# Kernel tuning notes

Measured on AMD Instinct MI355X. Metric: run time of the kernel, lower is better.

## Reference

```python
import jax, jax.numpy as jnp
import numpy as np

H = 16  # n_heads

def _rmsnorm(x, g, eps=1e-6):
    return x * jax.lax.rsqrt(jnp.mean(x * x, axis=-1, keepdims=True) + eps) * g

def _rope_diag(L, hd, dtype):
    # Diagonal of the full [L, hd, hd] rotary matrix: cos(pos * theta_pair) at every dim.
    # (The torch einsum 'bhld,ldd->bhld' extracts this diagonal, so no pairwise rotation occurs.)
    pair = jnp.arange(hd) // 2
    theta = 10000.0 ** (-2.0 * pair / hd)
    return jnp.cos(jnp.arange(L)[:, None].astype(jnp.float32) * theta[None, :]).astype(dtype)


def setup_inputs() -> dict:
    key = jax.random.key(0)
    ks = jax.random.split(key, 8)
    B, L, E = 2, 2048, 2048
    F = 2 * E  # SwiGLU width
    s = 0.02
    return {
        "x": jax.random.normal(ks[0], (B, L, E), jnp.float32),
        "g": jnp.ones((E,), jnp.float32),
        "wq": jax.random.normal(ks[1], (E, E), jnp.float32) * s,
        "wk": jax.random.normal(ks[2], (E, E), jnp.float32) * s,
        "wv": jax.random.normal(ks[3], (E, E), jnp.float32) * s,
        "w1": jax.random.normal(ks[4], (E, F), jnp.float32) * s,
        "b1": jnp.zeros((F,), jnp.float32),
        "wg": jax.random.normal(ks[5], (F, F), jnp.float32) * s,
        "bg": jnp.zeros((F,), jnp.float32),
        "wl": jax.random.normal(ks[6], (F, F), jnp.float32) * s,
        "bl": jnp.zeros((F,), jnp.float32),
        "beta": jnp.ones((1,), jnp.float32),
        "w2": jax.random.normal(ks[7], (F, E), jnp.float32) * s,
        "b2": jnp.zeros((E,), jnp.float32),
    }


def reference(x, g, wq, wk, wv, w1, b1, wg, bg, wl, bl, beta, w2, b2):
    B, L, E = x.shape
    hd = E // H
    x_res = x
    h = _rmsnorm(x, g)
    # projections -> [B, H, L, hd]
    q = (h @ wq).reshape(B, L, H, hd).transpose(0, 2, 1, 3)
    k = (h @ wk).reshape(B, L, H, hd).transpose(0, 2, 1, 3)
    v = (h @ wv).reshape(B, L, H, hd).transpose(0, 2, 1, 3)
    D = _rope_diag(L, hd, x.dtype)  # [L, hd], diagonal of rotary matrix
    q = q * D
    k = k * D
    score = jnp.einsum('bhld,bhmd->bhlm', q, k)  # [B,H,L,L]
    # causal mask added BEFORE scaling (faithful to source)
    mask = jnp.triu(jnp.full((L, L), -jnp.inf, dtype=score.dtype), k=1)
    score = (score + mask) / jnp.sqrt(jnp.asarray(hd, score.dtype))
    attn = jax.nn.softmax(score, axis=-1)
    o = jnp.einsum('bhlm,bhmd->bhld', attn, v)
    o = o.transpose(0, 2, 1, 3).reshape(B, L, E)
    x = o + x_res
    x_res = x
    h = _rmsnorm(x, g)
    h = h @ w1 + b1  # [B, L, 2E]
    gate = h @ wg + bg
    lin = h @ wl + bl
    act = gate * jax.nn.sigmoid(beta * gate) * lin
    out = act @ w2 + b2
    return out + x_res
```

## Files before the change

### kernel.cpp

```cpp
#include <hip/hip_runtime.h>
#include <cstdint>
#include <math.h>


typedef _Float16 f16;
typedef _Float16 f16x8 __attribute__((ext_vector_type(8)));
typedef _Float16 f16x4 __attribute__((ext_vector_type(4)));
typedef float    f32x4 __attribute__((ext_vector_type(4)));

#define MFMA_16x16x32(a, b, c) __builtin_amdgcn_mfma_f32_16x16x32_f16(a, b, c, 0, 0, 0)

__device__ __forceinline__ void gload_lds16(const void* g, void* lds) {
  __builtin_amdgcn_global_load_lds(
      (__attribute__((address_space(1))) void*)(uintptr_t)g,
      (__attribute__((address_space(3))) void*)(unsigned)(uintptr_t)lds,
      16, 0, 0);
}

__global__ void convT_k(const float* __restrict__ W, f16* __restrict__ Wt,
                        int K, int N) {
  __shared__ float tile[32][33];
  const int n0 = blockIdx.x << 5, k0 = blockIdx.y << 5;
  const int t = threadIdx.x;
  const int r = t >> 3, c4 = (t & 7) << 2;
  const f32x4 v = *(const f32x4*)(W + (size_t)(k0 + r) * N + n0 + c4);
  tile[r][c4 + 0] = v[0]; tile[r][c4 + 1] = v[1];
  tile[r][c4 + 2] = v[2]; tile[r][c4 + 3] = v[3];
  __syncthreads();
  f16x4 o;
  o[0] = (f16)tile[c4 + 0][r]; o[1] = (f16)tile[c4 + 1][r];
  o[2] = (f16)tile[c4 + 2][r]; o[3] = (f16)tile[c4 + 3][r];
  *(f16x4*)(Wt + (size_t)(n0 + r) * K + k0 + c4) = o;
}

__global__ void rope_tab_k(float* __restrict__ Dt) {
  const int l = blockIdx.x, d = threadIdx.x;
  const float th = __expf(-0.0719557841f * (float)(d & ~1));
  Dt[(l << 7) + d] = cosf((float)l * th);
}

__global__ void rmsnorm_k(const float* __restrict__ X, const float* __restrict__ G,
                          f16* __restrict__ H) {
  __shared__ float red[4];
  const int row = blockIdx.x, t = threadIdx.x;
  const float* xp = X + ((size_t)row << 11) + (t << 3);
  const f32x4 v0 = *(const f32x4*)xp;
  const f32x4 v1 = *(const f32x4*)(xp + 4);
  float ss = v0[0]*v0[0] + v0[1]*v0[1] + v0[2]*v0[2] + v0[3]*v0[3]
           + v1[0]*v1[0] + v1[1]*v1[1] + v1[2]*v1[2] + v1[3]*v1[3];
#pragma unroll
  for (int m = 1; m < 64; m <<= 1) ss += __shfl_xor(ss, m);
  if ((t & 63) == 0) red[t >> 6] = ss;
  __syncthreads();
  const float tot = red[0] + red[1] + red[2] + red[3];
  const float rs = rsqrtf(tot * (1.f / 2048.f) + 1e-6f);
  const float* gp = G + (t << 3);
  const f32x4 g0 = *(const f32x4*)gp, g1 = *(const f32x4*)(gp + 4);
  f16x8 o;
  o[0] = (f16)(v0[0]*rs*g0[0]); o[1] = (f16)(v0[1]*rs*g0[1]);
  o[2] = (f16)(v0[2]*rs*g0[2]); o[3] = (f16)(v0[3]*rs*g0[3]);
  o[4] = (f16)(v1[0]*rs*g1[0]); o[5] = (f16)(v1[1]*rs*g1[1]);
  o[6] = (f16)(v1[2]*rs*g1[2]); o[7] = (f16)(v1[3]*rs*g1[3]);
  *(f16x8*)(H + ((size_t)row << 11) + (t << 3)) = o;
}

__global__ void vtrans_k(const f16* __restrict__ V, f16* __restrict__ Vt) {
  __shared__ f16 tile[32][36];
  const int l0 = blockIdx.x << 5, d0 = blockIdx.y << 5, bh = blockIdx.z;
  const int b = bh >> 4, h = bh & 15;
  const int t = threadIdx.x;
  const int r = t >> 3, c4 = (t & 7) << 2;
  const f16x4 v = *(const f16x4*)(V + (size_t)((b << 11) + l0 + r) * 2048 + (h << 7) + d0 + c4);
  tile[r][c4 + 0] = v[0]; tile[r][c4 + 1] = v[1];
  tile[r][c4 + 2] = v[2]; tile[r][c4 + 3] = v[3];
  __syncthreads();
  f16x4 o;
  o[0] = tile[c4 + 0][r]; o[1] = tile[c4 + 1][r];
  o[2] = tile[c4 + 2][r]; o[3] = tile[c4 + 3][r];
  *(f16x4*)(Vt + (size_t)((bh << 7) + d0 + r) * 2048 + l0 + c4) = o;
}

template <int EPI>
__launch_bounds__(512, 2)
__global__ void gemm256_k(const f16* __restrict__ A, const f16* __restrict__ Bt,
                          void* __restrict__ Cout, int M, int N, int K,
                          const float* __restrict__ bias,
                          const f16* __restrict__ auxh,
                          const float* __restrict__ betap) {
  __shared__ alignas(16) f16 lds[65536];
  const int t = threadIdx.x, lane = t & 63, w = t >> 6;
  const int wm = w >> 2, wn = w & 3;
  const int bm = blockIdx.y << 8, bn = blockIdx.x << 8;
  const int lh = lane & 15, lq = lane >> 4;
  const int NT = K >> 6;
  const int lrow = lane >> 3;
  const int lco  = ((lane & 7) ^ lrow) << 3;

  const f16* Agl = A  + (size_t)(bm + lrow) * K + lco;
  const f16* Bgl = Bt + (size_t)(bn + lrow) * K + lco;
  const int aw = w << 3;
  const int bw = w << 4;

  f32x4 acc[8][4] = {};
  f16x8 bf[4][2];

  auto stA = [&](int tile, int half) {
    const int d = (tile & 1) << 15;
    const int k0 = tile << 6;
    const int r0 = aw + (half << 6);
    gload_lds16(Agl + (size_t)r0 * K + k0, (void*)&lds[d + r0 * 64]);
    gload_lds16(Agl + (size_t)(r0 + 128) * K + k0, (void*)&lds[d + (r0 + 128) * 64]);
  };
  auto stB = [&](int tile, int half) {
    const int d = ((tile & 1) << 15) + 16384;
    const int k0 = tile << 6;
    const int r0 = bw + (half << 7);
    gload_lds16(Bgl + (size_t)r0 * K + k0, (void*)&lds[d + r0 * 64]);
    gload_lds16(Bgl + (size_t)(r0 + 8) * K + k0, (void*)&lds[d + (r0 + 8) * 64]);
  };
  auto ldA = [&](int d, int mi, int kk) {
    const int r = (wm << 7) + (mi << 4) + lh;
    return *(const f16x8*)&lds[(d << 15) + r * 64 + ((((kk << 2) + lq) ^ (lh & 7)) << 3)];
  };
  auto ldB = [&](int d, int ni, int kk) {
    const int r = (wn << 6) + (ni << 4) + lh;
    return *(const f16x8*)&lds[(d << 15) + 16384 + r * 64 + ((((kk << 2) + lq) ^ (lh & 7)) << 3)];
  };

  stB(0, 0); stB(0, 1); stA(0, 0); stA(0, 1);
  stB(1, 0); stB(1, 1); stA(1, 0);
  asm volatile("s_waitcnt vmcnt(6)" ::: "memory");
  __builtin_amdgcn_s_barrier();

  for (int tt = 0; tt < NT; tt += 2) {
    const bool pf = (tt + 2 < NT);
#pragma unroll
    for (int hf = 0; hf < 2; ++hf) {
#pragma unroll
      for (int ph = 0; ph < 4; ++ph) {
        f16x8 a0k0 = ldA(hf, 2 * ph, 0),     a0k1 = ldA(hf, 2 * ph, 1);
        f16x8 a1k0 = ldA(hf, 2 * ph + 1, 0), a1k1 = ldA(hf, 2 * ph + 1, 1);
        if (ph == 0) {
#pragma unroll
          for (int ni = 0; ni < 4; ++ni) {
            bf[ni][0] = ldB(hf, ni, 0); bf[ni][1] = ldB(hf, ni, 1);
          }
        }
        if (hf == 0) {
          if (ph == 0) stA(tt + 1, 1);
          else if (ph == 1) { if (pf) stB(tt + 2, 0); }
          else if (ph == 2) { if (pf) stB(tt + 2, 1); }
          else              { if (pf) stA(tt + 2, 0); }
        } else {
          if (ph == 0)      { if (pf) stA(tt + 2, 1); }
          else if (ph == 1) { if (pf) stB(tt + 3, 0); }
          else if (ph == 2) { if (pf) stB(tt + 3, 1); }
          else              { if (pf) stA(tt + 3, 0); }
        }
        __builtin_amdgcn_s_barrier();
        __builtin_amdgcn_s_setprio(1);
#pragma unroll
        for (int ni = 0; ni < 4; ++ni) {
          acc[2 * ph][ni]     = MFMA_16x16x32(a0k0, bf[ni][0], acc[2 * ph][ni]);
          acc[2 * ph][ni]     = MFMA_16x16x32(a0k1, bf[ni][1], acc[2 * ph][ni]);
          acc[2 * ph + 1][ni] = MFMA_16x16x32(a1k0, bf[ni][0], acc[2 * ph + 1][ni]);
          acc[2 * ph + 1][ni] = MFMA_16x16x32(a1k1, bf[ni][1], acc[2 * ph + 1][ni]);
        }
        __builtin_amdgcn_s_setprio(0);
        if (ph == 3) {
          if (hf == 0) {
            if (pf) asm volatile("s_waitcnt vmcnt(6)" ::: "memory");
            else    asm volatile("s_waitcnt vmcnt(0)" ::: "memory");
          } else if (pf) {
            asm volatile("s_waitcnt vmcnt(6)" ::: "memory");
          }
        }
        __builtin_amdgcn_s_barrier();
      }
    }
  }

  const float be = (EPI == 3) ? betap[0] : 0.f;
#pragma unroll
  for (int mi = 0; mi < 8; ++mi) {
#pragma unroll
    for (int ni = 0; ni < 4; ++ni) {
#pragma unroll
      for (int r = 0; r < 4; ++r) {
        const int grow = bm + (wm << 7) + (mi << 4) + (lq << 2) + r;
        const int gcol = bn + (wn << 6) + (ni << 4) + lh;
        float v = acc[mi][ni][r] + bias[gcol];
        const size_t off = (size_t)grow * N + gcol;
        if (EPI == 2) {
          ((f16*)Cout)[off] = (f16)v;
        } else if (EPI == 3) {
          ((f16*)Cout)[off] = (f16)(v / (1.f + __expf(-be * v)));
        } else {
          ((f16*)Cout)[off] = (f16)(v * (float)auxh[off]);
        }
      }
    }
  }
}

template <int EPI>
__launch_bounds__(256, 2)
__global__ void gemm_k(const f16* __restrict__ A, const f16* __restrict__ Bt,
                       void* __restrict__ Cout, int M, int N, int K,
                       const float* __restrict__ bias,
                       const float* __restrict__ auxf,
                       float scale) {
  __shared__ alignas(16) f16 As[128 * 64];
  __shared__ alignas(16) f16 Bs[128 * 64];
  const int t = threadIdx.x;
  const int lane = t & 63;
  const int w = t >> 6;
  const int wm = w >> 1, wn = w & 1;
  const int bm = blockIdx.y << 7;
  const int bn = blockIdx.x << 7;
  const int lh = lane & 15, lq = lane >> 4;

  f32x4 acc[4][4] = {};

  for (int k0 = 0; k0 < K; k0 += 64) {
    __syncthreads();
#pragma unroll
    for (int i = 0; i < 4; ++i) {
      const int idx = i * 256 + (w << 6) + lane;
      const int row = idx >> 3, c = idx & 7;
      const int cs = (c ^ (row & 7)) << 3;
      gload_lds16(A + (size_t)(bm + row) * K + k0 + cs,
                  &As[(i * 256 + (w << 6)) << 3]);
      gload_lds16(Bt + (size_t)(bn + row) * K + k0 + cs,
                  &Bs[(i * 256 + (w << 6)) << 3]);
    }
    asm volatile("s_waitcnt vmcnt(0)" ::: "memory");
    __syncthreads();
#pragma unroll
    for (int kk = 0; kk < 2; ++kk) {
      f16x8 af[4], bfr[4];
#pragma unroll
      for (int mi = 0; mi < 4; ++mi) {
        const int r = (wm << 6) + (mi << 4) + lh;
        af[mi] = *(const f16x8*)&As[(r << 6) + ((((kk << 2) + lq) ^ (r & 7)) << 3)];
      }
#pragma unroll
      for (int ni = 0; ni < 4; ++ni) {
        const int r = (wn << 6) + (ni << 4) + lh;
        bfr[ni] = *(const f16x8*)&Bs[(r << 6) + ((((kk << 2) + lq) ^ (r & 7)) << 3)];
      }
#pragma unroll
      for (int mi = 0; mi < 4; ++mi)
#pragma unroll
        for (int ni = 0; ni < 4; ++ni)
          acc[mi][ni] = MFMA_16x16x32(af[mi], bfr[ni], acc[mi][ni]);
    }
  }

#pragma unroll
  for (int mi = 0; mi < 4; ++mi) {
#pragma unroll
    for (int ni = 0; ni < 4; ++ni) {
#pragma unroll
      for (int r = 0; r < 4; ++r) {
        const int grow = bm + (wm << 6) + (mi << 4) + (lq << 2) + r;
        const int gcol = bn + (wn << 6) + (ni << 4) + lh;
        float v = acc[mi][ni][r];
        const size_t off = (size_t)grow * N + gcol;
        if (EPI == 0) {
          v *= scale * auxf[((grow & 2047) << 7) + (gcol & 127)];
          ((f16*)Cout)[off] = (f16)v;
        } else if (EPI == 1) {
          ((f16*)Cout)[off] = (f16)v;
        } else {
          ((float*)Cout)[off] = v + bias[gcol] + auxf[off];
        }
      }
    }
  }
}

__launch_bounds__(256, 2)
__global__ void attn_k(const f16* __restrict__ Q, const f16* __restrict__ Kb,
                       const f16* __restrict__ Vt, const float* __restrict__ Xres,
                       float* __restrict__ X2, int* __restrict__ qcnt) {
  constexpr int L = 2048, E = 2048, HD = 128;
  __shared__ alignas(16) f16 Ks[2][64 * 128];
  __shared__ alignas(16) f16 Vs[128 * 64];
  __shared__ alignas(16) f16 Ps[4][32 * 72];
  __shared__ int s_item;

  const int t = threadIdx.x, lane = t & 63, w = t >> 6;
  const int lh = lane & 15, lq = lane >> 4;

  for (;;) {
    if (t == 0) s_item = atomicAdd(qcnt, 1);
    __syncthreads();
    const int item = s_item;
    if (item >= 512) return;
    const int bh = item & 31;
    const int q0 = (15 - (item >> 5)) << 7;
    const int b = bh >> 4, h = bh & 15;
    const int wrow0 = q0 + (w << 5);

    auto issueK = [&](int kv0, int buf) {
#pragma unroll
      for (int i = 0; i < 4; ++i) {
        const int idx = i * 256 + (w << 6) + lane;
        const int row = idx >> 4, c = idx & 15;
        gload_lds16(Kb + (size_t)(b * L + kv0 + row) * E + h * HD + ((c ^ (row & 7)) << 3),
                    &Ks[buf][(i * 256 + (w << 6)) << 3]);
      }
    };
    auto issueV = [&](int kv0) {
#pragma unroll
      for (int i = 0; i < 4; ++i) {
        const int idx = i * 256 + (w << 6) + lane;
        const int row = idx >> 3, c = idx & 7;
        gload_lds16(Vt + ((size_t)bh * HD + row) * L + kv0 + ((c ^ (row & 7)) << 3),
                    &Vs[(i * 256 + (w << 6)) << 3]);
      }
    };

    f16x8 qf[2][4];
#pragma unroll
    for (int mi = 0; mi < 2; ++mi) {
      const f16* qrow = Q + (size_t)(b * L + wrow0 + (mi << 4) + lh) * E + h * HD;
#pragma unroll
      for (int kq = 0; kq < 4; ++kq)
        qf[mi][kq] = *(const f16x8*)(qrow + (kq << 5) + (lq << 3));
    }
    asm volatile("s_waitcnt vmcnt(0)" ::: "memory");

    f32x4 oacc[2][8] = {};
    float mrun[2][4], lrun[2][4];
#pragma unroll
    for (int mi = 0; mi < 2; ++mi)
#pragma unroll
      for (int r = 0; r < 4; ++r) { mrun[mi][r] = -1e30f; lrun[mi][r] = 0.f; }

    const int nt = (q0 + 128) >> 6;
    issueK(0, 0);
    for (int it = 0; it < nt; ++it) {
      const int cur = it & 1;
      const int kv0 = it << 6;
      const bool more = (it + 1 < nt);
      issueV(kv0);
      if (more) {
        issueK(kv0 + 64, cur ^ 1);
        asm volatile("s_waitcnt vmcnt(8)" ::: "memory");
      } else {
        asm volatile("s_waitcnt vmcnt(4)" ::: "memory");
      }
      __builtin_amdgcn_s_barrier();

      const bool active = (kv0 <= wrow0 + 31);
      if (active) {
        f32x4 sacc[2][4] = {};
#pragma unroll
        for (int kq = 0; kq < 4; ++kq) {
          f16x8 kf[4];
#pragma unroll
          for (int ni = 0; ni < 4; ++ni) {
            const int r = (ni << 4) + lh;
            kf[ni] = *(const f16x8*)&Ks[cur][(r << 7) + ((((kq << 2) + lq) ^ (r & 7)) << 3)];
          }
#pragma unroll
          for (int mi = 0; mi < 2; ++mi)
#pragma unroll
            for (int ni = 0; ni < 4; ++ni)
              sacc[mi][ni] = MFMA_16x16x32(qf[mi][kq], kf[ni], sacc[mi][ni]);
        }
        if (kv0 + 63 > wrow0) {
#pragma unroll
          for (int mi = 0; mi < 2; ++mi)
#pragma unroll
            for (int ni = 0; ni < 4; ++ni)
#pragma unroll
              for (int r = 0; r < 4; ++r) {
                const int qr = wrow0 + (mi << 4) + (lq << 2) + r;
                const int kv = kv0 + (ni << 4) + lh;
                if (kv > qr) sacc[mi][ni][r] = -1e30f;
              }
        }
        float scl[2][4], rsum[2][4];
#pragma unroll
        for (int mi = 0; mi < 2; ++mi)
#pragma unroll
          for (int r = 0; r < 4; ++r) {
            float v = fmaxf(fmaxf(sacc[mi][0][r], sacc[mi][1][r]),
                            fmaxf(sacc[mi][2][r], sacc[mi][3][r]));
            v = fmaxf(v, __shfl_xor(v, 1));
            v = fmaxf(v, __shfl_xor(v, 2));
            v = fmaxf(v, __shfl_xor(v, 4));
            v = fmaxf(v, __shfl_xor(v, 8));
            const float mnew = fmaxf(mrun[mi][r], v);
            scl[mi][r] = __expf(mrun[mi][r] - mnew);
            mrun[mi][r] = mnew;
            rsum[mi][r] = 0.f;
          }
#pragma unroll
        for (int mi = 0; mi < 2; ++mi)
#pragma unroll
          for (int ni = 0; ni < 4; ++ni)
#pragma unroll
            for (int r = 0; r < 4; ++r) {
              const float p = __expf(sacc[mi][ni][r] - mrun[mi][r]);
              rsum[mi][r] += p;
              Ps[w][((mi << 4) + (lq << 2) + r) * 72 + (ni << 4) + lh] = (f16)p;
            }
#pragma unroll
        for (int mi = 0; mi < 2; ++mi)
#pragma unroll
          for (int r = 0; r < 4; ++r) {
            float s = rsum[mi][r];
            s += __shfl_xor(s, 1);
            s += __shfl_xor(s, 2);
            s += __shfl_xor(s, 4);
            s += __shfl_xor(s, 8);
            lrun[mi][r] = lrun[mi][r] * scl[mi][r] + s;
          }
#pragma unroll
        for (int mi = 0; mi < 2; ++mi)
#pragma unroll
          for (int nd = 0; nd < 8; ++nd)
#pragma unroll
            for (int r = 0; r < 4; ++r) oacc[mi][nd][r] *= scl[mi][r];
      }

      if (more) asm volatile("s_waitcnt vmcnt(4)" ::: "memory");
      else      asm volatile("s_waitcnt vmcnt(0)" ::: "memory");
      __builtin_amdgcn_s_barrier();

      if (active) {
#pragma unroll
        for (int kp = 0; kp < 2; ++kp) {
          f16x8 pf[2];
#pragma unroll
          for (int mi = 0; mi < 2; ++mi)
            pf[mi] = *(const f16x8*)&Ps[w][((mi << 4) + lh) * 72 + (kp << 5) + (lq << 3)];
#pragma unroll
          for (int nd = 0; nd < 8; ++nd) {
            const int r = (nd << 4) + lh;
            const f16x8 vf = *(const f16x8*)&Vs[(r << 6) + ((((kp << 2) + lq) ^ (r & 7)) << 3)];
#pragma unroll
            for (int mi = 0; mi < 2; ++mi)
              oacc[mi][nd] = MFMA_16x16x32(pf[mi], vf, oacc[mi][nd]);
          }
        }
      }
      asm volatile("" ::: "memory");
      __builtin_amdgcn_s_barrier();
    }
#pragma unroll
    for (int mi = 0; mi < 2; ++mi)
#pragma unroll
      for (int nd = 0; nd < 8; ++nd)
#pragma unroll
        for (int r = 0; r < 4; ++r) {
          const int qr = wrow0 + (mi << 4) + (lq << 2) + r;
          const size_t off = (size_t)(b * L + qr) * E + h * HD + (nd << 4) + lh;
          X2[off] = oacc[mi][nd][r] / lrun[mi][r] + Xres[off];
        }
  }
}

extern "C" void kernel_launch(void* const* d_in, const int* in_sizes, int n_in,
                              void* d_out, int out_size, void* d_ws, size_t ws_size,
                              hipStream_t stream) {
  const float* x    = (const float*)d_in[0];
  const float* g    = (const float*)d_in[1];
  const float* wq   = (const float*)d_in[2];
  const float* wk   = (const float*)d_in[3];
  const float* wv   = (const float*)d_in[4];
  const float* w1   = (const float*)d_in[5];
  const float* b1   = (const float*)d_in[6];
  const float* wgp  = (const float*)d_in[7];
  const float* bg   = (const float*)d_in[8];
  const float* wl   = (const float*)d_in[9];
  const float* bl   = (const float*)d_in[10];
  const float* beta = (const float*)d_in[11];
  const float* w2   = (const float*)d_in[12];
  const float* b2   = (const float*)d_in[13];

  constexpr size_t MB = 1ull << 20;
  char* ws = (char*)d_ws;
  f16*   wT   = (f16*)(ws + 0 * MB);
  int*   qcnt = (int*)(ws + 31 * MB);
  float* Dt   = (float*)(ws + 32 * MB);
  f16*   hbuf = (f16*)(ws + 33 * MB);
  f16*   qbuf = (f16*)(ws + 49 * MB);
  f16*   kbuf = (f16*)(ws + 65 * MB);
  f16*   vbuf = (f16*)(ws + 81 * MB);
  f16*   vtb  = (f16*)(ws + 97 * MB);
  float* x2   = (float*)(ws + 113 * MB);
  f16*   a1   = (f16*)(ws + 49 * MB);
  f16*   sbuf = (f16*)(ws + 81 * MB);
  f16*   act  = (f16*)(ws + 145 * MB);
  (void)ws_size; (void)n_in; (void)in_sizes; (void)out_size;

  const dim3 blk(256);
  const float qscale = 0.08838834764831845f;

  rope_tab_k<<<2048, 128, 0, stream>>>(Dt);
  rmsnorm_k<<<4096, blk, 0, stream>>>(x, g, hbuf);
  hipMemsetAsync(qcnt, 0, 4, stream);

  f16* wqT = wT;
  f16* wkT = wT + (size_t)2048 * 2048;
  f16* wvT = wT + (size_t)4096 * 2048;
  convT_k<<<dim3(64, 64), blk, 0, stream>>>(wq, wqT, 2048, 2048);
  convT_k<<<dim3(64, 64), blk, 0, stream>>>(wk, wkT, 2048, 2048);
  convT_k<<<dim3(64, 64), blk, 0, stream>>>(wv, wvT, 2048, 2048);
  gemm_k<0><<<dim3(16, 32), blk, 0, stream>>>(hbuf, wqT, qbuf, 4096, 2048, 2048,
                                              nullptr, Dt, qscale);
  gemm_k<0><<<dim3(16, 32), blk, 0, stream>>>(hbuf, wkT, kbuf, 4096, 2048, 2048,
                                              nullptr, Dt, 1.0f);
  gemm_k<1><<<dim3(16, 32), blk, 0, stream>>>(hbuf, wvT, vbuf, 4096, 2048, 2048,
                                              nullptr, nullptr, 1.0f);
  vtrans_k<<<dim3(64, 4, 32), blk, 0, stream>>>(vbuf, vtb);

  attn_k<<<384, blk, 0, stream>>>(qbuf, kbuf, vtb, x, x2, qcnt);

  rmsnorm_k<<<4096, blk, 0, stream>>>(x2, g, hbuf);

  convT_k<<<dim3(128, 64), blk, 0, stream>>>(w1, wT, 2048, 4096);
  gemm256_k<2><<<dim3(16, 16), 512, 0, stream>>>(hbuf, wT, a1, 4096, 4096, 2048,
                                                 b1, nullptr, nullptr);
  convT_k<<<dim3(128, 128), blk, 0, stream>>>(wgp, wT, 4096, 4096);
  gemm256_k<3><<<dim3(16, 16), 512, 0, stream>>>(a1, wT, sbuf, 4096, 4096, 4096,
                                                 bg, nullptr, beta);
  convT_k<<<dim3(128, 128), blk, 0, stream>>>(wl, wT, 4096, 4096);
  gemm256_k<4><<<dim3(16, 16), 512, 0, stream>>>(a1, wT, act, 4096, 4096, 4096,
                                                 bl, sbuf, nullptr);
  convT_k<<<dim3(64, 128), blk, 0, stream>>>(w2, wT, 4096, 2048);
  gemm_k<5><<<dim3(16, 32), blk, 0, stream>>>(act, wT, (float*)d_out, 4096, 2048, 4096,
                                              b2, x2, 1.0f);
}
```

Measured before the change: 727.1 us.

## Store attention residual in fp16, add fp16 RMSNorm, move gate-linear GEMM to 128-tile kernel

The post-attention residual x2 is now written as fp16 instead of fp32, and a new RMSNorm kernel reads fp16 input. The final GEMM reads that fp16 residual, which halves the traffic for writing and re-reading the residual. The fused SwiGLU linear GEMM moves from the 256-tile kernel to the 128-tile gemm_k with a new epilogue, and gemm_k's launch bounds go from 2 to 3 blocks per SM. Storing the residual in fp16 loses precision in the skip path that feeds the output.

```diff
diff --git a/kernel.cpp b/kernel.cpp
--- a/kernel.cpp
+++ b/kernel.cpp
@@ -61,6 +61,33 @@
   o[2] = (f16)(v0[2]*rs*g0[2]); o[3] = (f16)(v0[3]*rs*g0[3]);
   o[4] = (f16)(v1[0]*rs*g1[0]); o[5] = (f16)(v1[1]*rs*g1[1]);
   o[6] = (f16)(v1[2]*rs*g1[2]); o[7] = (f16)(v1[3]*rs*g1[3]);
+  *(f16x8*)(H + ((size_t)row << 11) + (t << 3)) = o;
+}
+
+__global__ void rmsnorm_h_k(const f16* __restrict__ X, const float* __restrict__ G,
+                            f16* __restrict__ H) {
+  __shared__ float red[4];
+  const int row = blockIdx.x, t = threadIdx.x;
+  const f16x8 v = *(const f16x8*)(X + ((size_t)row << 11) + (t << 3));
+  float f[8];
+#pragma unroll
+  for (int i = 0; i < 8; ++i) f[i] = (float)v[i];
+  float ss = 0.f;
+#pragma unroll
+  for (int i = 0; i < 8; ++i) ss += f[i] * f[i];
+#pragma unroll
+  for (int m = 1; m < 64; m <<= 1) ss += __shfl_xor(ss, m);
+  if ((t & 63) == 0) red[t >> 6] = ss;
+  __syncthreads();
+  const float tot = red[0] + red[1] + red[2] + red[3];
+  const float rs = rsqrtf(tot * (1.f / 2048.f) + 1e-6f);
+  const float* gp = G + (t << 3);
+  const f32x4 g0 = *(const f32x4*)gp, g1 = *(const f32x4*)(gp + 4);
+  f16x8 o;
+#pragma unroll
+  for (int i = 0; i < 4; ++i) o[i] = (f16)(f[i] * rs * g0[i]);
+#pragma unroll
+  for (int i = 0; i < 4; ++i) o[4 + i] = (f16)(f[4 + i] * rs * g1[i]);
   *(f16x8*)(H + ((size_t)row << 11) + (t << 3)) = o;
 }
 
@@ -204,11 +231,12 @@
 }
 
 template <int EPI>
-__launch_bounds__(256, 2)
+__launch_bounds__(256, 3)
 __global__ void gemm_k(const f16* __restrict__ A, const f16* __restrict__ Bt,
                        void* __restrict__ Cout, int M, int N, int K,
                        const float* __restrict__ bias,
                        const float* __restrict__ auxf,
+                       const f16* __restrict__ auxh,
                        float scale) {
   __shared__ alignas(16) f16 As[128 * 64];
   __shared__ alignas(16) f16 Bs[128 * 64];
@@ -272,8 +300,10 @@
           ((f16*)Cout)[off] = (f16)v;
         } else if (EPI == 1) {
           ((f16*)Cout)[off] = (f16)v;
+        } else if (EPI == 4) {
+          ((f16*)Cout)[off] = (f16)((v + bias[gcol]) * (float)auxh[off]);
         } else {
-          ((float*)Cout)[off] = v + bias[gcol] + auxf[off];
+          ((float*)Cout)[off] = v + bias[gcol] + (float)auxh[off];
         }
       }
     }
@@ -283,7 +313,7 @@
 __launch_bounds__(256, 2)
 __global__ void attn_k(const f16* __restrict__ Q, const f16* __restrict__ Kb,
                        const f16* __restrict__ Vt, const float* __restrict__ Xres,
-                       float* __restrict__ X2, int* __restrict__ qcnt) {
+                       f16* __restrict__ X2, int* __restrict__ qcnt) {
   constexpr int L = 2048, E = 2048, HD = 128;
   __shared__ alignas(16) f16 Ks[2][64 * 128];
   __shared__ alignas(16) f16 Vs[128 * 64];
@@ -460,7 +490,7 @@
         for (int r = 0; r < 4; ++r) {
           const int qr = wrow0 + (mi << 4) + (lq << 2) + r;
           const size_t off = (size_t)(b * L + qr) * E + h * HD + (nd << 4) + lh;
-          X2[off] = oacc[mi][nd][r] / lrun[mi][r] + Xres[off];
+          X2[off] = (f16)(oacc[mi][nd][r] / lrun[mi][r] + Xres[off]);
         }
   }
 }
@@ -493,7 +523,7 @@
   f16*   kbuf = (f16*)(ws + 65 * MB);
   f16*   vbuf = (f16*)(ws + 81 * MB);
   f16*   vtb  = (f16*)(ws + 97 * MB);
-  float* x2   = (float*)(ws + 113 * MB);
+  f16*   x2h  = (f16*)(ws + 113 * MB);
   f16*   a1   = (f16*)(ws + 49 * MB);
   f16*   sbuf = (f16*)(ws + 81 * MB);
   f16*   act  = (f16*)(ws + 145 * MB);
@@ -513,16 +543,16 @@
   convT_k<<<dim3(64, 64), blk, 0, stream>>>(wk, wkT, 2048, 2048);
   convT_k<<<dim3(64, 64), blk, 0, stream>>>(wv, wvT, 2048, 2048);
   gemm_k<0><<<dim3(16, 32), blk, 0, stream>>>(hbuf, wqT, qbuf, 4096, 2048, 2048,
-                                              nullptr, Dt, qscale);
+                                              nullptr, Dt, nullptr, qscale);
   gemm_k<0><<<dim3(16, 32), blk, 0, stream>>>(hbuf, wkT, kbuf, 4096, 2048, 2048,
-                                              nullptr, Dt, 1.0f);
+                                              nullptr, Dt, nullptr, 1.0f);
   gemm_k<1><<<dim3(16, 32), blk, 0, stream>>>(hbuf, wvT, vbuf, 4096, 2048, 2048,
-                                              nullptr, nullptr, 1.0f);
+                                              nullptr, nullptr, nullptr, 1.0f);
   vtrans_k<<<dim3(64, 4, 32), blk, 0, stream>>>(vbuf, vtb);
 
-  attn_k<<<384, blk, 0, stream>>>(qbuf, kbuf, vtb, x, x2, qcnt);
-
-  rmsnorm_k<<<4096, blk, 0, stream>>>(x2, g, hbuf);
+  attn_k<<<384, blk, 0, stream>>>(qbuf, kbuf, vtb, x, x2h, qcnt);
+
+  rmsnorm_h_k<<<4096, blk, 0, stream>>>(x2h, g, hbuf);
 
   convT_k<<<dim3(128, 64), blk, 0, stream>>>(w1, wT, 2048, 4096);
   gemm256_k<2><<<dim3(16, 16), 512, 0, stream>>>(hbuf, wT, a1, 4096, 4096, 2048,
@@ -531,9 +561,9 @@
   gemm256_k<3><<<dim3(16, 16), 512, 0, stream>>>(a1, wT, sbuf, 4096, 4096, 4096,
                                                  bg, nullptr, beta);
   convT_k<<<dim3(128, 128), blk, 0, stream>>>(wl, wT, 4096, 4096);
-  gemm256_k<4><<<dim3(16, 16), 512, 0, stream>>>(a1, wT, act, 4096, 4096, 4096,
-                                                 bl, sbuf, nullptr);
+  gemm_k<4><<<dim3(32, 32), blk, 0, stream>>>(a1, wT, act, 4096, 4096, 4096,
+                                              bl, nullptr, sbuf, 1.0f);
   convT_k<<<dim3(64, 128), blk, 0, stream>>>(w2, wT, 4096, 2048);
   gemm_k<5><<<dim3(16, 32), blk, 0, stream>>>(act, wT, (float*)d_out, 4096, 2048, 4096,
-                                              b2, x2, 1.0f);
-}
+                                              b2, nullptr, x2h, 1.0f);
+}
```

After: 728.2 us. No clear change (+0.2%).
